# Performance work log

Measured on AMD Instinct MI355X. Metric: run time of the kernel, lower is better.

Reference implementation:

```python
import jax, jax.numpy as jnp
import numpy as np

FEATURE_STRIDE = 16
CFG = {"TRAIN": dict(pre=12000, post=2000, thresh=0.7, min_size=16.0),
       "TEST":  dict(pre=6000,  post=300,  thresh=0.7, min_size=16.0)}

def _generate_anchors(base_size=16, ratios=(0.5, 1.0, 2.0), scales=(8, 16, 32)):
    xc = yc = (base_size - 1) * 0.5
    size = float(base_size * base_size)
    out = []
    for r in ratios:
        w = np.round(np.sqrt(size / r))
        h = np.round(w * r)
        for s in scales:
            W, H = w * s, h * s
            out.append([xc - 0.5 * (W - 1), yc - 0.5 * (H - 1),
                        xc + 0.5 * (W - 1), yc + 0.5 * (H - 1)])
    return np.array(out, np.float32)

ANCHORS = jnp.asarray(_generate_anchors())  # (9, 4)
NUM_ANCHORS = ANCHORS.shape[0]

def _pairwise_iou(b):
    x1, y1, x2, y2 = b[:, 0], b[:, 1], b[:, 2], b[:, 3]
    area = (x2 - x1 + 1.0) * (y2 - y1 + 1.0)
    iw = jnp.clip(jnp.minimum(x2[:, None], x2[None]) - jnp.maximum(x1[:, None], x1[None]) + 1.0, 0.0)
    ih = jnp.clip(jnp.minimum(y2[:, None], y2[None]) - jnp.maximum(y1[:, None], y1[None]) + 1.0, 0.0)
    inter = iw * ih
    return inter / (area[:, None] + area[None] - inter)

def _nms_keep(boxes, valid, thresh):
    # greedy NMS over score-sorted boxes; returns bool keep mask
    K = boxes.shape[0]
    iou = _pairwise_iou(boxes)  # (K, K)
    rng = jnp.arange(K)
    def body(i, keep):
        conflict = jnp.any((rng < i) & keep & (iou[i] > thresh))
        return keep.at[i].set(valid[i] & ~conflict)
    return jax.lax.fori_loop(0, K, body, jnp.zeros((K,), bool))

def reference(rpn_cls_scores, rpn_bbox_adjusts, img_shapes, train):
    cfg = CFG["TRAIN" if train else "TEST"]
    B, _, H, W = rpn_cls_scores.shape
    A = NUM_ANCHORS
    # fg scores: channels [A:2A], layout (h, w, a) after permute
    scores = rpn_cls_scores[:, A:].transpose(0, 2, 3, 1).reshape(B, -1)      # (B, N)
    deltas = rpn_bbox_adjusts.transpose(0, 2, 3, 1).reshape(B, -1, 4)        # (B, N, 4)
    # all anchors on the feature grid
    sx = jnp.arange(W, dtype=jnp.float32) * FEATURE_STRIDE
    sy = jnp.arange(H, dtype=jnp.float32) * FEATURE_STRIDE
    gy, gx = jnp.meshgrid(sy, sx, indexing="ij")
    shifts = jnp.stack([gx, gy, gx, gy], -1).reshape(-1, 4)                  # (H*W, 4)
    anchors = (shifts[:, None, :] + ANCHORS[None]).reshape(-1, 4)            # (N, 4)
    # bbox_transform_inv (+1 convention)
    aw = anchors[:, 2] - anchors[:, 0] + 1.0
    ah = anchors[:, 3] - anchors[:, 1] + 1.0
    acx = anchors[:, 0] + 0.5 * aw
    acy = anchors[:, 1] + 0.5 * ah
    pcx = deltas[..., 0] * aw + acx
    pcy = deltas[..., 1] * ah + acy
    pw = jnp.exp(deltas[..., 2]) * aw
    ph = jnp.exp(deltas[..., 3]) * ah
    x1, y1 = pcx - 0.5 * pw, pcy - 0.5 * ph
    x2, y2 = pcx + 0.5 * pw, pcy + 0.5 * ph
    imh, imw = img_shapes[:, 0:1], img_shapes[:, 1:2]
    x1 = jnp.clip(x1, 0.0, imw - 1.0); x2 = jnp.clip(x2, 0.0, imw - 1.0)
    y1 = jnp.clip(y1, 0.0, imh - 1.0); y2 = jnp.clip(y2, 0.0, imh - 1.0)
    boxes = jnp.stack([x1, y1, x2, y2], -1)                                  # (B, N, 4)
    valid = ((x2 - x1 + 1.0) >= cfg["min_size"]) & ((y2 - y1 + 1.0) >= cfg["min_size"])
    masked = jnp.where(valid, scores, -jnp.inf)
    K = min(cfg["pre"], boxes.shape[1])
    top_s, idx = jax.lax.top_k(masked, K)                                    # (B, K)
    top_b = jnp.take_along_axis(boxes, idx[..., None], axis=1)               # (B, K, 4)
    keep = jax.vmap(lambda b, v: _nms_keep(b, v, cfg["thresh"]))(
        jax.lax.stop_gradient(top_b), jnp.isfinite(top_s))
    post = cfg["post"]
    fin_s = jnp.where(keep, top_s, -jnp.inf)
    sel_s, idx2 = jax.lax.top_k(fin_s, post)
    sel_b = jnp.take_along_axis(top_b, idx2[..., None], axis=1)              # (B, post, 4)
    sel_b = jnp.where(jnp.isfinite(sel_s)[..., None], sel_b, 0.0)
    bix = jnp.broadcast_to(jnp.arange(B, dtype=sel_b.dtype)[:, None, None], (B, post, 1))
    return jnp.concatenate([bix, sel_b], -1)                                 # (B, post, 5)

def setup_inputs():
    key = jax.random.key(0)
    k1, k2 = jax.random.split(key)
    B, H, W = 4, 64, 96
    rpn_cls_scores = jax.random.normal(k1, (B, 2 * NUM_ANCHORS, H, W), jnp.float32)
    rpn_bbox_adjusts = jax.random.normal(k2, (B, 4 * NUM_ANCHORS, H, W), jnp.float32) * 0.1
    img_shapes = jnp.tile(jnp.array([[1024.0, 1536.0]], jnp.float32), (B, 1))
    return {"rpn_cls_scores": rpn_cls_scores, "rpn_bbox_adjusts": rpn_bbox_adjusts,
            "img_shapes": img_shapes, "train": 0}
```

## Files before the change

### kernel.cpp

```cpp
#include <hip/hip_runtime.h>


#define NB 4
#define AH 64
#define AW 96
#define NA 9
#define NPOS (AH*AW)
#define NPC (NPOS*NA)
#define CAP 16384
#define PREMAX 12000
#define POSTMAX 2048
#define HBITS 15
#define HSZ (1<<HBITS)
#define HSH (32-HBITS)

__constant__ float c_anchors[NA][4] = {
  { -84.f,  -40.f,  99.f,  55.f},
  {-176.f,  -88.f, 191.f, 103.f},
  {-360.f, -184.f, 375.f, 199.f},
  { -56.f,  -56.f,  71.f,  71.f},
  {-120.f, -120.f, 135.f, 135.f},
  {-248.f, -248.f, 263.f, 263.f},
  { -36.f,  -80.f,  51.f,  95.f},
  { -80.f, -168.f,  95.f, 183.f},
  {-168.f, -344.f, 183.f, 359.f},
};

__device__ unsigned int       g_keys[NB][NPC];
__device__ float4             g_boxes[NB][NPC];
__device__ unsigned int       g_h15[NB][HSZ];
__device__ int                g_cnt[NB];
__device__ unsigned long long g_cand[NB][CAP];
__device__ int                g_cidx[NB][CAP];
__device__ int                g_rank[NB][CAP];
__device__ float4             g_sbox[NB][PREMAX];

__device__ __forceinline__ bool iou_gt(float4 a, float areaA, float4 q, float areaQ) {
#pragma clang fp contract(off)
  float iw = fminf(a.z, q.z) - fmaxf(a.x, q.x) + 1.0f; iw = fmaxf(iw, 0.0f);
  float ih = fminf(a.w, q.w) - fmaxf(a.y, q.y) + 1.0f; ih = fmaxf(ih, 0.0f);
  float inter = iw * ih;
  float denom = areaA + areaQ - inter;
  float d = inter - 0.7f * denom;
  if (__builtin_expect(fabsf(d) <= 4e-6f * denom, 0))
    return (inter / denom) > 0.7f;
  return d > 0.0f;
}

__global__ void __launch_bounds__(256)
k1_decode(const float* __restrict__ cls, const float* __restrict__ dlt,
          const float* __restrict__ ish) {
#pragma clang fp contract(off)
  const int UPB = NPOS/256;
  int bid = blockIdx.x;
  int b   = bid / (NA*UPB);
  int r   = bid % (NA*UPB);
  int a   = r / UPB;
  int pos = (r % UPB) * 256 + threadIdx.x;
  int i2  = a * NPOS + pos;

  int wx = pos % AW;
  int hy = pos / AW;

  float score = cls[(b * (2*NA) + NA + a) * NPOS + pos];
  const float* dp = dlt + (b * (4*NA) + a*4) * NPOS + pos;
  float d0 = dp[0];
  float d1 = dp[NPOS];
  float d2 = dp[2*NPOS];
  float d3 = dp[3*NPOS];

  float shx = (float)(wx * 16);
  float shy = (float)(hy * 16);
  float ax1 = c_anchors[a][0] + shx;
  float ay1 = c_anchors[a][1] + shy;
  float ax2 = c_anchors[a][2] + shx;
  float ay2 = c_anchors[a][3] + shy;

  float aw_ = ax2 - ax1 + 1.0f;
  float ah_ = ay2 - ay1 + 1.0f;
  float acx = ax1 + 0.5f * aw_;
  float acy = ay1 + 0.5f * ah_;

  float pcx = d0 * aw_ + acx;
  float pcy = d1 * ah_ + acy;
  float pw  = expf(d2) * aw_;
  float ph  = expf(d3) * ah_;

  float x1 = pcx - 0.5f * pw;
  float y1 = pcy - 0.5f * ph;
  float x2 = pcx + 0.5f * pw;
  float y2 = pcy + 0.5f * ph;

  float imh = ish[b*2 + 0];
  float imw = ish[b*2 + 1];
  x1 = fminf(fmaxf(x1, 0.0f), imw - 1.0f);
  x2 = fminf(fmaxf(x2, 0.0f), imw - 1.0f);
  y1 = fminf(fmaxf(y1, 0.0f), imh - 1.0f);
  y2 = fminf(fmaxf(y2, 0.0f), imh - 1.0f);

  bool valid = ((x2 - x1 + 1.0f) >= 16.0f) && ((y2 - y1 + 1.0f) >= 16.0f);

  g_boxes[b][i2] = make_float4(x1, y1, x2, y2);

  unsigned int key = 0u;
  if (valid) {
    unsigned int ub = __float_as_uint(score);
    key = (ub >> 31) ? ~ub : (ub | 0x80000000u);
  }
  g_keys[b][i2] = key;
  atomicAdd(&g_h15[b][key >> HSH], 1u);
}

__global__ void __launch_bounds__(1024)
k2_pivcmp(const int* __restrict__ train) {
  const int UPB = NPOS/1024;
  int tid = threadIdx.x;
  int bid = blockIdx.x;
  int b   = bid / (NA*UPB);
  int r   = bid % (NA*UPB);
  int a   = r / UPB;
  int pos = (r % UPB) * 1024 + tid;
  int i2  = a * NPOS + pos;
  unsigned int pre = train[0] ? 12000u : 6000u;

  __shared__ unsigned int csum[1024];
  __shared__ unsigned int c32[32];
  __shared__ unsigned int c32s[33];
  __shared__ int sBest;

  const int CH = HSZ / 1024;
  unsigned int hb[CH];
  const uint4* hp = (const uint4*)&g_h15[b][tid * CH];
#pragma unroll
  for (int q = 0; q < CH/4; ++q) {
    uint4 v = hp[q];
    hb[4*q+0] = v.x; hb[4*q+1] = v.y; hb[4*q+2] = v.z; hb[4*q+3] = v.w;
  }
  unsigned int s = 0;
#pragma unroll
  for (int q = 0; q < CH; ++q) s += hb[q];
  csum[tid] = s;
  if (tid == 0) sBest = 0;
  __syncthreads();
  if (tid < 32) {
    unsigned int ss = 0;
    for (int q = 0; q < 32; ++q) ss += csum[tid*32 + q];
    c32[tid] = ss;
  }
  __syncthreads();
  if (tid == 0) {
    unsigned int run = 0; c32s[32] = 0;
    for (int c = 31; c >= 0; --c) { run += c32[c]; c32s[c] = run; }
  }
  __syncthreads();
  unsigned int run = c32s[(tid >> 5) + 1];
  for (int t2 = (tid | 31); t2 > tid; --t2) run += csum[t2];
  int loc = 0;
#pragma unroll
  for (int q = CH-1; q >= 0; --q) {
    run += hb[q];
    if (!loc && run >= pre) {
      int T = tid * CH + q;
      if (T >= 1) loc = T;
    }
  }
  if (loc) atomicMax(&sBest, loc);
  __syncthreads();
  unsigned int pivot = sBest ? ((unsigned int)sBest << HSH) : 1u;

  unsigned int key = g_keys[b][i2];
  if (key >= pivot) {
    int p = atomicAdd(&g_cnt[b], 1);
    if (p < CAP) {
      unsigned int iref = (unsigned int)(pos * NA + a);
      g_cand[b][p] = ((unsigned long long)key << 32) |
                     (unsigned long long)(0xFFFFFFFFu - iref);
      g_cidx[b][p] = i2;
    }
  }
}

__global__ void __launch_bounds__(256) k3_rank() {
  int tid = threadIdx.x;
  __shared__ unsigned long long tl[256];
  for (int b = 0; b < NB; ++b) {
    int C = g_cnt[b]; if (C > CAP) C = CAP;
    int nt = (C + 255) >> 8;
    int tiles = nt * nt;
    for (int t = blockIdx.x; t < tiles; t += gridDim.x) {
      int jt = t / nt, kt = t - jt * nt;
      int k = kt * 256 + tid;
      tl[tid] = (k < C) ? g_cand[b][k] : 0ull;
      __syncthreads();
      int j = jt * 256 + tid;
      unsigned long long cj = (j < C) ? g_cand[b][j] : ~0ull;
      int rk = 0;
#pragma unroll 8
      for (int q = 0; q < 256; ++q) rk += (int)(tl[q] > cj);
      if (j < C && rk) atomicAdd(&g_rank[b][j], rk);
      __syncthreads();
    }
  }
}

__global__ void __launch_bounds__(1024)
k4_nms(float* __restrict__ out, const int* __restrict__ train, int post) {
#pragma clang fp contract(off)
  int bid = blockIdx.x;
  int tid = threadIdx.x;

  if (bid >= NB) {
    uint4* hz = (uint4*)g_h15;
    const int total = NB*HSZ/4;
    for (int idx = (bid - NB) * 1024 + tid; idx < total; idx += 28*1024)
      hz[idx] = make_uint4(0u, 0u, 0u, 0u);
    return;
  }

  int b = bid;
  int lane = tid & 63;
  int wid  = tid >> 6;
  int pre = train[0] ? 12000 : 6000;

  __shared__ float4 kbox[POSTMAX];
  __shared__ float  kar [POSTMAX];
  __shared__ float4 cbox[64];
  __shared__ float  car [64];
  __shared__ unsigned long long conf16[16][64];
  __shared__ unsigned long long sup16[16];
  __shared__ int s_nk;
  __shared__ int s_cb;

  if (tid == 0) {
    int c = g_cnt[b];
    g_cnt[b] = 0;
    s_cb = (c > CAP) ? CAP : c;
    s_nk = 0;
  }
  __syncthreads();
  int Cb = s_cb;
  int Kb = min(pre, Cb);

  for (int j = tid; j < Cb; j += 1024) {
    int rkk = g_rank[b][j];
    g_rank[b][j] = 0;
    if (rkk < pre) g_sbox[b][rkk] = g_boxes[b][g_cidx[b][j]];
  }
  __syncthreads();

  if (wid == 15) {
    float4 bx0 = (lane < Kb) ? g_sbox[b][lane] : make_float4(0.f,0.f,-1.f,-1.f);
    cbox[lane] = bx0;
    car[lane]  = (bx0.z - bx0.x + 1.0f) * (bx0.w - bx0.y + 1.0f);
  }
  __syncthreads();

  int nk = 0;
  unsigned long long laneBitsBelow = (lane == 0) ? 0ull : (~0ull >> (64 - lane));

  for (int base = 0; base < Kb; base += 64) {
    float4 bx  = cbox[lane];
    float area = car[lane];
    bool active = (base + lane < Kb);

    float4 nxt = make_float4(0.f, 0.f, -1.f, -1.f);
    if (wid == 15) {
      int c2 = base + 64 + lane;
      if (c2 < Kb) nxt = g_sbox[b][c2];
    }

    int supp = active ? 0 : 1;
    {
      int t = wid;
      for (; t + 48 < nk; t += 64) {
        supp |= (int)iou_gt(bx, area, kbox[t],    kar[t]);
        supp |= (int)iou_gt(bx, area, kbox[t+16], kar[t+16]);
        supp |= (int)iou_gt(bx, area, kbox[t+32], kar[t+32]);
        supp |= (int)iou_gt(bx, area, kbox[t+48], kar[t+48]);
      }
      for (; t < nk; t += 16) supp |= (int)iou_gt(bx, area, kbox[t], kar[t]);
    }
    unsigned long long sb = __ballot(supp);
    if (lane == 0) sup16[wid] = sb;

    {
      unsigned long long confp = 0ull;
#pragma unroll
      for (int q = 0; q < 4; ++q) {
        int j = (wid << 2) + q;
        if (iou_gt(bx, area, cbox[j], car[j])) confp |= (1ull << j);
      }
      conf16[wid][lane] = confp;
    }
    __syncthreads();

    if (wid == 0) {
      unsigned long long conf = 0ull;
#pragma unroll
      for (int w = 0; w < 16; ++w) conf |= conf16[w][lane];
      conf &= laneBitsBelow;
      unsigned long long supAll = 0ull;
#pragma unroll
      for (int w = 0; w < 16; ++w) supAll |= sup16[w];
      unsigned long long pending = ~supAll;
      unsigned long long keptmask = 0ull;
      while (pending) {
        int i = __ffsll(pending) - 1;
        keptmask |= (1ull << i);
        unsigned long long confb = __ballot((int)((conf >> i) & 1ull));
        pending &= ~confb;
        pending &= ~(1ull << i);
      }
      int myPos = nk + __popcll(keptmask & laneBitsBelow);
      if (((keptmask >> lane) & 1ull) && myPos < post) {
        kbox[myPos] = bx;
        kar [myPos] = area;
        float* o = out + ((size_t)b * post + myPos) * 5;
        o[0] = (float)b; o[1] = bx.x; o[2] = bx.y; o[3] = bx.z; o[4] = bx.w;
      }
      if (lane == 0) s_nk = nk + __popcll(keptmask);
    } else if (wid == 15) {
      cbox[lane] = nxt;
      car[lane]  = (nxt.z - nxt.x + 1.0f) * (nxt.w - nxt.y + 1.0f);
    }
    __syncthreads();
    nk = s_nk;
    if (nk >= post) break;
  }

  nk = min(nk, post);
  for (int rr = nk + tid; rr < post; rr += 1024) {
    float* o = out + ((size_t)b * post + rr) * 5;
    o[0] = (float)b; o[1] = 0.0f; o[2] = 0.0f; o[3] = 0.0f; o[4] = 0.0f;
  }
}

extern "C" void kernel_launch(void* const* d_in, const int* in_sizes, int n_in,
                              void* d_out, int out_size, void* d_ws, size_t ws_size,
                              hipStream_t stream) {
  (void)in_sizes; (void)n_in; (void)d_ws; (void)ws_size;
  const float* cls   = (const float*)d_in[0];
  const float* dlt   = (const float*)d_in[1];
  const float* ish   = (const float*)d_in[2];
  const int*   train = (const int*)d_in[3];
  float* out = (float*)d_out;

  int post = out_size / (NB * 5);

  k1_decode<<<NB*NA*(NPOS/256), 256, 0, stream>>>(cls, dlt, ish);
  k2_pivcmp<<<NB*NA*(NPOS/1024), 1024, 0, stream>>>(train);
  k3_rank<<<1024, 256, 0, stream>>>();
  k4_nms<<<32, 1024, 0, stream>>>(out, train, post);
}
```

Baseline: 172.2 us.

## Fuse pivot, compaction, bitonic sort in LDS and NMS into one per-image kernel

Replaces the pivot/compaction kernel, the O(C^2) pairwise rank kernel and the NMS kernel with a single kernel that uses one 1024-thread block per image. Each block finds the histogram pivot, compacts candidates into 64 KB of shared memory, bitonic-sorts 8192 keys in LDS, gathers the top boxes and runs the same NMS. It also clears its own histogram slice at the end. This removes two launches and the quadratic ranking work, but leaves only 4 blocks for the compaction and sort, so most of the GPU sits idle. Candidates are now capped at 8192 instead of 16384.

Result: slower. 215.5 us (+25.1%).

```diff
diff --git a/kernel.cpp b/kernel.cpp
--- a/kernel.cpp
+++ b/kernel.cpp
@@ -7,12 +7,12 @@
 #define NA 9
 #define NPOS (AH*AW)
 #define NPC (NPOS*NA)
-#define CAP 16384
-#define PREMAX 12000
+#define LDSN 8192
 #define POSTMAX 2048
 #define HBITS 15
 #define HSZ (1<<HBITS)
 #define HSH (32-HBITS)
+#define NTHR 1024
 
 __constant__ float c_anchors[NA][4] = {
   { -84.f,  -40.f,  99.f,  55.f},
@@ -26,14 +26,11 @@
   {-168.f, -344.f, 183.f, 359.f},
 };
 
-__device__ unsigned int       g_keys[NB][NPC];
-__device__ float4             g_boxes[NB][NPC];
-__device__ unsigned int       g_h15[NB][HSZ];
-__device__ int                g_cnt[NB];
-__device__ unsigned long long g_cand[NB][CAP];
-__device__ int                g_cidx[NB][CAP];
-__device__ int                g_rank[NB][CAP];
-__device__ float4             g_sbox[NB][PREMAX];
+__device__ unsigned int g_keys[NB][NPC];
+__device__ float4       g_boxes[NB][NPC];
+__device__ unsigned int g_h15[NB][HSZ];
+__device__ int          g_cnt[NB];
+__device__ float4       g_sbox[NB][LDSN];
 
 __device__ __forceinline__ bool iou_gt(float4 a, float areaA, float4 q, float areaQ) {
 #pragma clang fp contract(off)
@@ -48,7 +45,7 @@
 }
 
 __global__ void __launch_bounds__(256)
-k1_decode(const float* __restrict__ cls, const float* __restrict__ dlt,
+kA_decode(const float* __restrict__ cls, const float* __restrict__ dlt,
           const float* __restrict__ ish) {
 #pragma clang fp contract(off)
   const int UPB = NPOS/256;
@@ -111,227 +108,211 @@
   atomicAdd(&g_h15[b][key >> HSH], 1u);
 }
 
-__global__ void __launch_bounds__(1024)
-k2_pivcmp(const int* __restrict__ train) {
-  const int UPB = NPOS/1024;
-  int tid = threadIdx.x;
-  int bid = blockIdx.x;
-  int b   = bid / (NA*UPB);
-  int r   = bid % (NA*UPB);
-  int a   = r / UPB;
-  int pos = (r % UPB) * 1024 + tid;
-  int i2  = a * NPOS + pos;
-  unsigned int pre = train[0] ? 12000u : 6000u;
-
-  __shared__ unsigned int csum[1024];
-  __shared__ unsigned int c32[32];
-  __shared__ unsigned int c32s[33];
-  __shared__ int sBest;
-
-  const int CH = HSZ / 1024;
-  unsigned int hb[CH];
-  const uint4* hp = (const uint4*)&g_h15[b][tid * CH];
-#pragma unroll
-  for (int q = 0; q < CH/4; ++q) {
-    uint4 v = hp[q];
-    hb[4*q+0] = v.x; hb[4*q+1] = v.y; hb[4*q+2] = v.z; hb[4*q+3] = v.w;
-  }
-  unsigned int s = 0;
-#pragma unroll
-  for (int q = 0; q < CH; ++q) s += hb[q];
-  csum[tid] = s;
-  if (tid == 0) sBest = 0;
+__global__ void __launch_bounds__(NTHR)
+kB_sortnms(float* __restrict__ out, const int* __restrict__ train, int post) {
+#pragma clang fp contract(off)
+  const int tid = threadIdx.x;
+  const int b   = blockIdx.x;
+  const int pre = train[0] ? 12000 : 6000;
+
+  __shared__ __align__(16) unsigned char smem[65536];
+
+  unsigned int pivot;
+  {
+    unsigned int* csum = (unsigned int*)smem;
+    unsigned int* c32  = (unsigned int*)(smem + 4096);
+    unsigned int* c32s = (unsigned int*)(smem + 4224);
+    int* sBest         = (int*)(smem + 4360);
+
+    const int CH = HSZ / NTHR;
+    unsigned int hb[CH];
+    const uint4* hp = (const uint4*)&g_h15[b][tid * CH];
+#pragma unroll
+    for (int q = 0; q < CH/4; ++q) {
+      uint4 v = hp[q];
+      hb[4*q+0] = v.x; hb[4*q+1] = v.y; hb[4*q+2] = v.z; hb[4*q+3] = v.w;
+    }
+    unsigned int s = 0;
+#pragma unroll
+    for (int q = 0; q < CH; ++q) s += hb[q];
+    csum[tid] = s;
+    if (tid == 0) *sBest = 0;
+    __syncthreads();
+    if (tid < 32) {
+      unsigned int ss = 0;
+      for (int q = 0; q < 32; ++q) ss += csum[tid*32 + q];
+      c32[tid] = ss;
+    }
+    __syncthreads();
+    if (tid == 0) {
+      unsigned int run = 0; c32s[32] = 0;
+      for (int c = 31; c >= 0; --c) { run += c32[c]; c32s[c] = run; }
+    }
+    __syncthreads();
+    unsigned int run = c32s[(tid >> 5) + 1];
+    for (int t2 = (tid | 31); t2 > tid; --t2) run += csum[t2];
+    int loc = 0;
+#pragma unroll
+    for (int q = CH-1; q >= 0; --q) {
+      run += hb[q];
+      if (!loc && run >= (unsigned)pre) {
+        int T = tid * CH + q;
+        if (T >= 1) loc = T;
+      }
+    }
+    if (loc) atomicMax(sBest, loc);
+    __syncthreads();
+    pivot = (*sBest) ? ((unsigned int)(*sBest) << HSH) : 1u;
+  }
   __syncthreads();
-  if (tid < 32) {
-    unsigned int ss = 0;
-    for (int q = 0; q < 32; ++q) ss += csum[tid*32 + q];
-    c32[tid] = ss;
+
+  unsigned long long* sl = (unsigned long long*)smem;
+  for (int i2 = tid; i2 < NPC; i2 += NTHR) {
+    unsigned int key = g_keys[b][i2];
+    if (key >= pivot) {
+      int p = atomicAdd(&g_cnt[b], 1);
+      if (p < LDSN) {
+        int a = i2 / NPOS, pos = i2 - a * NPOS;
+        unsigned int iref = (unsigned int)(pos * NA + a);
+        sl[p] = ((unsigned long long)key << 32) |
+                (unsigned long long)(0xFFFFFFFFu - iref);
+      }
+    }
   }
   __syncthreads();
-  if (tid == 0) {
-    unsigned int run = 0; c32s[32] = 0;
-    for (int c = 31; c >= 0; --c) { run += c32[c]; c32s[c] = run; }
-  }
+  int C = __hip_atomic_load(&g_cnt[b], __ATOMIC_RELAXED, __HIP_MEMORY_SCOPE_AGENT);
+  if (C > LDSN) C = LDSN;
+  for (int p = C + tid; p < LDSN; p += NTHR) sl[p] = 0ull;
   __syncthreads();
-  unsigned int run = c32s[(tid >> 5) + 1];
-  for (int t2 = (tid | 31); t2 > tid; --t2) run += csum[t2];
-  int loc = 0;
-#pragma unroll
-  for (int q = CH-1; q >= 0; --q) {
-    run += hb[q];
-    if (!loc && run >= pre) {
-      int T = tid * CH + q;
-      if (T >= 1) loc = T;
-    }
-  }
-  if (loc) atomicMax(&sBest, loc);
+
+  for (int k = 2; k <= LDSN; k <<= 1) {
+    for (int j = k >> 1; j > 0; j >>= 1) {
+#pragma unroll 4
+      for (int t = tid; t < LDSN/2; t += NTHR) {
+        int i   = ((t & ~(j - 1)) << 1) | (t & (j - 1));
+        int ixj = i + j;
+        unsigned long long A = sl[i], B = sl[ixj];
+        if ((A < B) == ((i & k) == 0)) { sl[i] = B; sl[ixj] = A; }
+      }
+      __syncthreads();
+    }
+  }
+
+  int Kb = min(pre, C);
+  for (int r = tid; r < Kb; r += NTHR) {
+    unsigned int iref = 0xFFFFFFFFu - (unsigned int)(sl[r] & 0xFFFFFFFFull);
+    int pos = iref / NA, a = iref - pos * NA;
+    g_sbox[b][r] = g_boxes[b][a * NPOS + pos];
+  }
   __syncthreads();
-  unsigned int pivot = sBest ? ((unsigned int)sBest << HSH) : 1u;
-
-  unsigned int key = g_keys[b][i2];
-  if (key >= pivot) {
-    int p = atomicAdd(&g_cnt[b], 1);
-    if (p < CAP) {
-      unsigned int iref = (unsigned int)(pos * NA + a);
-      g_cand[b][p] = ((unsigned long long)key << 32) |
-                     (unsigned long long)(0xFFFFFFFFu - iref);
-      g_cidx[b][p] = i2;
-    }
-  }
-}
-
-__global__ void __launch_bounds__(256) k3_rank() {
-  int tid = threadIdx.x;
-  __shared__ unsigned long long tl[256];
-  for (int b = 0; b < NB; ++b) {
-    int C = g_cnt[b]; if (C > CAP) C = CAP;
-    int nt = (C + 255) >> 8;
-    int tiles = nt * nt;
-    for (int t = blockIdx.x; t < tiles; t += gridDim.x) {
-      int jt = t / nt, kt = t - jt * nt;
-      int k = kt * 256 + tid;
-      tl[tid] = (k < C) ? g_cand[b][k] : 0ull;
+
+  {
+    float4* kbox = (float4*)smem;
+    float*  kar  = (float*)(smem + 32768);
+    float4* cbox = (float4*)(smem + 40960);
+    float*  car  = (float*)(smem + 41984);
+    unsigned long long (*conf16)[64] =
+        (unsigned long long (*)[64])(smem + 42240);
+    unsigned long long* sup16 =
+        (unsigned long long*)(smem + 50432);
+    int* s_nk = (int*)(smem + 50560);
+
+    int lane = tid & 63;
+    int wid  = tid >> 6;
+
+    if (tid == 0) *s_nk = 0;
+    if (wid == 15) {
+      float4 bx0 = (lane < Kb) ? g_sbox[b][lane] : make_float4(0.f,0.f,-1.f,-1.f);
+      cbox[lane] = bx0;
+      car[lane]  = (bx0.z - bx0.x + 1.0f) * (bx0.w - bx0.y + 1.0f);
+    }
+    __syncthreads();
+
+    int nk = 0;
+    unsigned long long laneBitsBelow = (lane == 0) ? 0ull : (~0ull >> (64 - lane));
+
+    for (int base = 0; base < Kb; base += 64) {
+      float4 bx  = cbox[lane];
+      float area = car[lane];
+      bool active = (base + lane < Kb);
+
+      float4 nxt = make_float4(0.f, 0.f, -1.f, -1.f);
+      if (wid == 15) {
+        int c2 = base + 64 + lane;
+        if (c2 < Kb) nxt = g_sbox[b][c2];
+      }
+
+      int supp = active ? 0 : 1;
+      {
+        int t = wid;
+        for (; t + 48 < nk; t += 64) {
+          supp |= (int)iou_gt(bx, area, kbox[t],    kar[t]);
+          supp |= (int)iou_gt(bx, area, kbox[t+16], kar[t+16]);
+          supp |= (int)iou_gt(bx, area, kbox[t+32], kar[t+32]);
+          supp |= (int)iou_gt(bx, area, kbox[t+48], kar[t+48]);
+        }
+        for (; t < nk; t += 16) supp |= (int)iou_gt(bx, area, kbox[t], kar[t]);
+      }
+      unsigned long long sb = __ballot(supp);
+      if (lane == 0) sup16[wid] = sb;
+
+      {
+        unsigned long long confp = 0ull;
+#pragma unroll
+        for (int q = 0; q < 4; ++q) {
+          int j = (wid << 2) + q;
+          if (iou_gt(bx, area, cbox[j], car[j])) confp |= (1ull << j);
+        }
+        conf16[wid][lane] = confp;
+      }
       __syncthreads();
-      int j = jt * 256 + tid;
-      unsigned long long cj = (j < C) ? g_cand[b][j] : ~0ull;
-      int rk = 0;
-#pragma unroll 8
-      for (int q = 0; q < 256; ++q) rk += (int)(tl[q] > cj);
-      if (j < C && rk) atomicAdd(&g_rank[b][j], rk);
+
+      if (wid == 0) {
+        unsigned long long conf = 0ull;
+#pragma unroll
+        for (int w = 0; w < 16; ++w) conf |= conf16[w][lane];
+        conf &= laneBitsBelow;
+        unsigned long long supAll = 0ull;
+#pragma unroll
+        for (int w = 0; w < 16; ++w) supAll |= sup16[w];
+        unsigned long long pending = ~supAll;
+        unsigned long long keptmask = 0ull;
+        while (pending) {
+          int i = __ffsll(pending) - 1;
+          keptmask |= (1ull << i);
+          unsigned long long confb = __ballot((int)((conf >> i) & 1ull));
+          pending &= ~confb;
+          pending &= ~(1ull << i);
+        }
+        int myPos = nk + __popcll(keptmask & laneBitsBelow);
+        if (((keptmask >> lane) & 1ull) && myPos < post) {
+          kbox[myPos] = bx;
+          kar [myPos] = area;
+          float* o = out + ((size_t)b * post + myPos) * 5;
+          o[0] = (float)b; o[1] = bx.x; o[2] = bx.y; o[3] = bx.z; o[4] = bx.w;
+        }
+        if (lane == 0) *s_nk = nk + __popcll(keptmask);
+      } else if (wid == 15) {
+        cbox[lane] = nxt;
+        car[lane]  = (nxt.z - nxt.x + 1.0f) * (nxt.w - nxt.y + 1.0f);
+      }
       __syncthreads();
-    }
-  }
-}
-
-__global__ void __launch_bounds__(1024)
-k4_nms(float* __restrict__ out, const int* __restrict__ train, int post) {
-#pragma clang fp contract(off)
-  int bid = blockIdx.x;
-  int tid = threadIdx.x;
-
-  if (bid >= NB) {
-    uint4* hz = (uint4*)g_h15;
-    const int total = NB*HSZ/4;
-    for (int idx = (bid - NB) * 1024 + tid; idx < total; idx += 28*1024)
-      hz[idx] = make_uint4(0u, 0u, 0u, 0u);
-    return;
-  }
-
-  int b = bid;
-  int lane = tid & 63;
-  int wid  = tid >> 6;
-  int pre = train[0] ? 12000 : 6000;
-
-  __shared__ float4 kbox[POSTMAX];
-  __shared__ float  kar [POSTMAX];
-  __shared__ float4 cbox[64];
-  __shared__ float  car [64];
-  __shared__ unsigned long long conf16[16][64];
-  __shared__ unsigned long long sup16[16];
-  __shared__ int s_nk;
-  __shared__ int s_cb;
-
-  if (tid == 0) {
-    int c = g_cnt[b];
-    g_cnt[b] = 0;
-    s_cb = (c > CAP) ? CAP : c;
-    s_nk = 0;
-  }
-  __syncthreads();
-  int Cb = s_cb;
-  int Kb = min(pre, Cb);
-
-  for (int j = tid; j < Cb; j += 1024) {
-    int rkk = g_rank[b][j];
-    g_rank[b][j] = 0;
-    if (rkk < pre) g_sbox[b][rkk] = g_boxes[b][g_cidx[b][j]];
-  }
-  __syncthreads();
-
-  if (wid == 15) {
-    float4 bx0 = (lane < Kb) ? g_sbox[b][lane] : make_float4(0.f,0.f,-1.f,-1.f);
-    cbox[lane] = bx0;
-    car[lane]  = (bx0.z - bx0.x + 1.0f) * (bx0.w - bx0.y + 1.0f);
-  }
-  __syncthreads();
-
-  int nk = 0;
-  unsigned long long laneBitsBelow = (lane == 0) ? 0ull : (~0ull >> (64 - lane));
-
-  for (int base = 0; base < Kb; base += 64) {
-    float4 bx  = cbox[lane];
-    float area = car[lane];
-    bool active = (base + lane < Kb);
-
-    float4 nxt = make_float4(0.f, 0.f, -1.f, -1.f);
-    if (wid == 15) {
-      int c2 = base + 64 + lane;
-      if (c2 < Kb) nxt = g_sbox[b][c2];
-    }
-
-    int supp = active ? 0 : 1;
-    {
-      int t = wid;
-      for (; t + 48 < nk; t += 64) {
-        supp |= (int)iou_gt(bx, area, kbox[t],    kar[t]);
-        supp |= (int)iou_gt(bx, area, kbox[t+16], kar[t+16]);
-        supp |= (int)iou_gt(bx, area, kbox[t+32], kar[t+32]);
-        supp |= (int)iou_gt(bx, area, kbox[t+48], kar[t+48]);
-      }
-      for (; t < nk; t += 16) supp |= (int)iou_gt(bx, area, kbox[t], kar[t]);
-    }
-    unsigned long long sb = __ballot(supp);
-    if (lane == 0) sup16[wid] = sb;
-
-    {
-      unsigned long long confp = 0ull;
-#pragma unroll
-      for (int q = 0; q < 4; ++q) {
-        int j = (wid << 2) + q;
-        if (iou_gt(bx, area, cbox[j], car[j])) confp |= (1ull << j);
-      }
-      conf16[wid][lane] = confp;
-    }
-    __syncthreads();
-
-    if (wid == 0) {
-      unsigned long long conf = 0ull;
-#pragma unroll
-      for (int w = 0; w < 16; ++w) conf |= conf16[w][lane];
-      conf &= laneBitsBelow;
-      unsigned long long supAll = 0ull;
-#pragma unroll
-      for (int w = 0; w < 16; ++w) supAll |= sup16[w];
-      unsigned long long pending = ~supAll;
-      unsigned long long keptmask = 0ull;
-      while (pending) {
-        int i = __ffsll(pending) - 1;
-        keptmask |= (1ull << i);
-        unsigned long long confb = __ballot((int)((conf >> i) & 1ull));
-        pending &= ~confb;
-        pending &= ~(1ull << i);
-      }
-      int myPos = nk + __popcll(keptmask & laneBitsBelow);
-      if (((keptmask >> lane) & 1ull) && myPos < post) {
-        kbox[myPos] = bx;
-        kar [myPos] = area;
-        float* o = out + ((size_t)b * post + myPos) * 5;
-        o[0] = (float)b; o[1] = bx.x; o[2] = bx.y; o[3] = bx.z; o[4] = bx.w;
-      }
-      if (lane == 0) s_nk = nk + __popcll(keptmask);
-    } else if (wid == 15) {
-      cbox[lane] = nxt;
-      car[lane]  = (nxt.z - nxt.x + 1.0f) * (nxt.w - nxt.y + 1.0f);
-    }
-    __syncthreads();
-    nk = s_nk;
-    if (nk >= post) break;
-  }
-
-  nk = min(nk, post);
-  for (int rr = nk + tid; rr < post; rr += 1024) {
-    float* o = out + ((size_t)b * post + rr) * 5;
-    o[0] = (float)b; o[1] = 0.0f; o[2] = 0.0f; o[3] = 0.0f; o[4] = 0.0f;
+      nk = *s_nk;
+      if (nk >= post) break;
+    }
+
+    nk = min(nk, post);
+    for (int rr = nk + tid; rr < post; rr += NTHR) {
+      float* o = out + ((size_t)b * post + rr) * 5;
+      o[0] = (float)b; o[1] = 0.0f; o[2] = 0.0f; o[3] = 0.0f; o[4] = 0.0f;
+    }
+  }
+
+  {
+    uint4* hz = (uint4*)&g_h15[b][0];
+    for (int q = tid; q < HSZ/4; q += NTHR) hz[q] = make_uint4(0u,0u,0u,0u);
+    if (tid == 0)
+      __hip_atomic_store(&g_cnt[b], 0, __ATOMIC_RELAXED, __HIP_MEMORY_SCOPE_AGENT);
   }
 }
 
@@ -347,8 +328,6 @@
 
   int post = out_size / (NB * 5);
 
-  k1_decode<<<NB*NA*(NPOS/256), 256, 0, stream>>>(cls, dlt, ish);
-  k2_pivcmp<<<NB*NA*(NPOS/1024), 1024, 0, stream>>>(train);
-  k3_rank<<<1024, 256, 0, stream>>>();
-  k4_nms<<<32, 1024, 0, stream>>>(out, train, post);
+  kA_decode<<<NB*NA*(NPOS/256), 256, 0, stream>>>(cls, dlt, ish);
+  kB_sortnms<<<NB, NTHR, 0, stream>>>(out, train, post);
 }
```
